# Kernel optimization log

Hardware: AMD Instinct MI355X
Metric: run time of the kernel (lower is better)

The kernel has to match this reference:

```python
import jax, jax.numpy as jnp
import numpy as np

B, T, V, D, E = 128, 50, 10000, 512, 2048


def setup_inputs() -> dict:
    key = jax.random.key(0)
    ks = jax.random.split(key, 14)
    s = 1.0 / np.sqrt(D)
    enc_out = jax.random.normal(ks[0], (B, E), jnp.float32)
    captions = jax.random.randint(ks[1], (B, T), 0, V)
    caplens = jax.random.randint(ks[2], (B, 1), 2, T + 1)
    caplens = caplens.at[0, 0].set(T)  # ensure max(caplens)-1 == T-1 (static shape)
    return {
        "enc_out": enc_out,
        "captions": captions,
        "caplens": caplens,
        "emb_W": jax.random.normal(ks[3], (V, D), jnp.float32),
        "W_ih": jax.random.uniform(ks[4], (4 * D, D), jnp.float32, -s, s),
        "W_hh": jax.random.uniform(ks[5], (4 * D, D), jnp.float32, -s, s),
        "b_ih": jax.random.uniform(ks[6], (4 * D,), jnp.float32, -s, s),
        "b_hh": jax.random.uniform(ks[7], (4 * D,), jnp.float32, -s, s),
        "fc_W": jax.random.uniform(ks[8], (V, D), jnp.float32, -s, s),
        "fc_b": jnp.zeros((V,), jnp.float32),
        "init_h_W": jax.random.uniform(ks[9], (D, E), jnp.float32, -s, s),
        "init_h_b": jnp.zeros((D,), jnp.float32),
        "init_c_W": jax.random.uniform(ks[10], (D, E), jnp.float32, -s, s),
        "init_c_b": jnp.zeros((D,), jnp.float32),
    }


def reference(enc_out, captions, caplens, emb_W, W_ih, W_hh, b_ih, b_hh,
              fc_W, fc_b, init_h_W, init_h_b, init_c_W, init_c_b):
    # Sort by caption length, descending (manual packing in the torch code).
    cl = caplens[:, 0]
    sort_idx = jnp.argsort(-cl)
    cl = cl[sort_idx]
    enc = enc_out[sort_idx]
    caps = captions[sort_idx]

    # init_states
    h0 = enc @ init_h_W.T + init_h_b  # [B, D]
    c0 = enc @ init_c_W.T + init_c_b

    emb = emb_W[caps]                  # [B, T, D] embedding gather
    dec_lens = cl - 1                  # decode lengths, max == T-1 by construction
    Tm = caps.shape[1] - 1             # static max timesteps

    # active-row mask per timestep: row b is active at step t iff t < dec_lens[b]
    masks = jnp.arange(Tm)[:, None] < dec_lens[None, :]   # [Tm, B]
    xs = jnp.moveaxis(emb[:, :Tm, :], 1, 0)               # [Tm, B, D]

    def step(carry, inp):
        h, c = carry
        x_t, m = inp                                      # [B,D], [B]
        gates = x_t @ W_ih.T + b_ih + h @ W_hh.T + b_hh   # [B, 4D]
        i, f, g, o = jnp.split(gates, 4, axis=-1)
        i = jax.nn.sigmoid(i)
        f = jax.nn.sigmoid(f)
        g = jnp.tanh(g)
        o = jax.nn.sigmoid(o)
        c_new = f * c + i * g
        h_new = o * jnp.tanh(c_new)
        mm = m[:, None]
        # inactive (shorter) rows keep their old state; torch never touches them
        h = jnp.where(mm, h_new, h)
        c = jnp.where(mm, c_new, c)
        # dropout in eval mode == identity; preds only written for active rows
        preds = jnp.where(mm, h_new @ fc_W.T + fc_b, 0.0)  # [B, V]
        return (h, c), preds

    (_, _), preds = jax.lax.scan(step, (h0, c0), (xs, masks))  # [Tm, B, V]
    predictions = jnp.moveaxis(preds, 0, 1)                    # [B, Tm, V]
    return predictions, caps, dec_lens, sort_idx
```

## Files before the change

### kernel.cpp

```cpp
#include <hip/hip_runtime.h>
#include <hip/hip_bf16.h>
#include <math.h>

typedef __attribute__((ext_vector_type(8))) short short8;
typedef __attribute__((ext_vector_type(4))) float f32x4;
typedef __attribute__((ext_vector_type(4))) unsigned short us4;
typedef unsigned short u16;
typedef unsigned long long u64;

#define TM 49
#define NV 10000
#define NLSTM 64
#define NFC 192
#define SMEM_BYTES 133120

__device__ __forceinline__ u16 f2bf(float f) {
    union { float f; unsigned u; } v; v.f = f;
    unsigned r = v.u + 0x7fffu + ((v.u >> 16) & 1u);
    return (u16)(r >> 16);
}
__device__ __forceinline__ float fsigm(float x) {
    return 1.0f / (1.0f + __expf(-x));
}
__device__ __forceinline__ float ftanh(float x) {
    float x2 = fminf(fmaxf(x + x, -30.0f), 30.0f);
    float e = __expf(x2);
    return (e - 1.0f) / (e + 1.0f);
}

__device__ __forceinline__ short8 ld_cp128(const u16* p) {
    short8 r;
    asm volatile("global_load_dwordx4 %0, %1, off sc0 sc1" : "=v"(r) : "v"(p));
    return r;
}
__device__ __forceinline__ void st_cp16(u16* p, unsigned v) {
    asm volatile("global_store_short %0, %1, off sc0 sc1" :: "v"(p), "v"(v) : "memory");
}
__device__ __forceinline__ void st_cp32f(float* p, float v) {
    asm volatile("global_store_dword %0, %1, off sc0 sc1" :: "v"(p), "v"(v) : "memory");
}
__device__ __forceinline__ unsigned ld_cp32_wait(const unsigned* p) {
    unsigned r;
    asm volatile("global_load_dword %0, %1, off sc0 sc1\n\ts_waitcnt vmcnt(0)"
                 : "=v"(r) : "v"(p) : "memory");
    return r;
}

__global__ __launch_bounds__(128) void k_sort(
    const int* __restrict__ caplens, const int* __restrict__ captions,
    const float* __restrict__ bih, const float* __restrict__ bhh,
    int* __restrict__ sidx, int* __restrict__ decl, int* __restrict__ capsS,
    float* __restrict__ bsum, float* __restrict__ out_tail,
    unsigned* __restrict__ slots, unsigned* __restrict__ xcnt,
    int* __restrict__ offs, int* __restrict__ rowmap, int* __restrict__ maskmap)
{
    __shared__ int s_cl[128];
    __shared__ int s_si[128];
    __shared__ int s_dl[128];
    __shared__ int s_n[49];
    __shared__ int s_off[50];
    __shared__ int s_moff[128];
    int tid = threadIdx.x;
    for (int k = tid; k < 256; k += 128)
        __hip_atomic_store(&slots[k], 0u, __ATOMIC_RELAXED, __HIP_MEMORY_SCOPE_AGENT);
    for (int k = tid; k < 1568; k += 128)
        __hip_atomic_store(&xcnt[k], 0u, __ATOMIC_RELAXED, __HIP_MEMORY_SCOPE_AGENT);
    int my = caplens[tid];
    s_cl[tid] = my;
    __syncthreads();
    int r = 0;
    for (int j = 0; j < 128; j++) {
        int cj = s_cl[j];
        if (cj > my || (cj == my && j < tid)) r++;
    }
    s_si[r] = tid;
    __syncthreads();
    int src = s_si[tid];
    sidx[tid] = src;
    int dl = s_cl[src] - 1;
    decl[tid] = dl;
    s_dl[tid] = dl;
    out_tail[6400 + tid] = (float)dl;
    out_tail[6528 + tid] = (float)src;
    for (int t = 0; t < 50; t++) {
        int tok = captions[src * 50 + t];
        capsS[tid * 50 + t] = tok;
        out_tail[tid * 50 + t] = (float)tok;
    }
    for (int k = tid; k < 2048; k += 128) bsum[k] = bih[k] + bhh[k];
    __syncthreads();
    if (tid < 49) {
        int c = 0;
        for (int b = 0; b < 128; b++) c += (s_dl[b] > tid);
        s_n[tid] = c;
    }
    __syncthreads();
    if (tid == 0) {
        int a = 0;
        for (int t = 0; t < 49; t++) { s_off[t] = a; a += s_n[t]; }
        s_off[49] = a;
        int m = 0;
        for (int b = 0; b < 128; b++) { s_moff[b] = m; m += 49 - s_dl[b]; }
    }
    __syncthreads();
    if (tid < 50) offs[tid] = s_off[tid];
    for (int t = 0; t < dl; t++) rowmap[s_off[t] + tid] = t * 128 + tid;
    int mo = s_moff[tid];
    for (int t = dl; t < 49; t++) maskmap[mo + (t - dl)] = tid * 49 + t;
}

__global__ __launch_bounds__(256) void k_cvt(
    const float* __restrict__ Wih, const float* __restrict__ Whh,
    const float* __restrict__ fcW, const float* __restrict__ ihW,
    const float* __restrict__ icW,
    u16* __restrict__ WihB, u16* __restrict__ WhhB,
    u16* __restrict__ fcWB, u16* __restrict__ WhcB)
{
    int idx = blockIdx.x * 256 + threadIdx.x;
    const float* src; u16* dst; int o;
    if (idx < 262144)        { src = Wih; dst = WihB; o = idx; }
    else if (idx < 524288)   { src = Whh; dst = WhhB; o = idx - 262144; }
    else if (idx < 1804288)  { src = fcW; dst = fcWB; o = idx - 524288; }
    else if (idx < 2066432)  { src = ihW; dst = WhcB; o = idx - 1804288; }
    else                     { src = icW; dst = WhcB + 1048576; o = idx - 2066432; }
    f32x4 v = *(const f32x4*)&src[(size_t)o * 4];
    us4 b = { f2bf(v.x), f2bf(v.y), f2bf(v.z), f2bf(v.w) };
    *(us4*)&dst[(size_t)o * 4] = b;
}

__global__ __launch_bounds__(256) void k_gather(
    const float* __restrict__ enc, const float* __restrict__ embW,
    const int* __restrict__ sidx, const int* __restrict__ capsS,
    u16* __restrict__ encB, u16* __restrict__ Xemb)
{
    int idx = blockIdx.x * 256 + threadIdx.x;
    if (idx < 65536) {
        int b = idx >> 9, k4 = idx & 511;
        f32x4 v = *(const f32x4*)&enc[(size_t)sidx[b] * 2048 + k4 * 4];
        us4 o = { f2bf(v.x), f2bf(v.y), f2bf(v.z), f2bf(v.w) };
        *(us4*)&encB[(size_t)b * 2048 + k4 * 4] = o;
    } else {
        int j = idx - 65536;
        int row = j >> 7, k4 = j & 127;
        int t = row >> 7, b = row & 127;
        int tok = capsS[b * 50 + t];
        f32x4 v = *(const f32x4*)&embW[(size_t)tok * 512 + k4 * 4];
        us4 o = { f2bf(v.x), f2bf(v.y), f2bf(v.z), f2bf(v.w) };
        *(us4*)&Xemb[(size_t)row * 512 + k4 * 4] = o;
    }
}

__device__ __forceinline__ void tile_gemm_plain(
    const u16* __restrict__ A, int lda, const u16* __restrict__ B, int ldb,
    int K, int tid, u16 (*As)[40], u16 (*Bs)[40], f32x4 acc[4][4])
{
    const int w = tid >> 6, l = tid & 63;
    const int wr = (w >> 1) * 64, wc = (w & 1) * 64;
    const int lr = l & 15, lg = l >> 4;
    for (int k0 = 0; k0 < K; k0 += 32) {
        __syncthreads();
        #pragma unroll
        for (int i = 0; i < 2; i++) {
            int L = tid * 8 + i * 2048;
            int r = L >> 5, c = L & 31;
            *(short8*)&As[r][c] = *(const short8*)&A[(size_t)r * lda + k0 + c];
            *(short8*)&Bs[r][c] = *(const short8*)&B[(size_t)r * ldb + k0 + c];
        }
        __syncthreads();
        short8 af[4], bfr[4];
        #pragma unroll
        for (int m = 0; m < 4; m++) af[m] = *(const short8*)&As[wr + m * 16 + lr][lg * 8];
        #pragma unroll
        for (int n = 0; n < 4; n++) bfr[n] = *(const short8*)&Bs[wc + n * 16 + lr][lg * 8];
        #pragma unroll
        for (int m = 0; m < 4; m++)
            #pragma unroll
            for (int n = 0; n < 4; n++)
                acc[m][n] = __builtin_amdgcn_mfma_f32_16x16x32_bf16(af[m], bfr[n], acc[m][n], 0, 0, 0);
    }
}

__global__ __launch_bounds__(256, 1) void lstm_fc(
    const u16* __restrict__ Whh, float* __restrict__ X,
    u16* __restrict__ hb0, u16* __restrict__ hb1,
    u16* __restrict__ HnewC,
    const int* __restrict__ decl, unsigned* __restrict__ slots,
    unsigned* __restrict__ xcnt,
    const int* __restrict__ offs, const int* __restrict__ rowmap,
    const int* __restrict__ maskmap,
    const u16* __restrict__ fcWB, const float* __restrict__ fcb,
    const u16* __restrict__ encB, const u16* __restrict__ WhcB,
    const u16* __restrict__ WihB, const u16* __restrict__ Xemb,
    const float* __restrict__ bsum,
    const float* __restrict__ ihb, const float* __restrict__ icb,
    float* __restrict__ out)
{
    extern __shared__ char smem[];
    const int tid = threadIdx.x;
    const int wg = blockIdx.x;

    if (wg < NLSTM) {
        u16 (*As)[520] = (u16(*)[520])smem;
        u16 (*Bsi)[520] = (u16(*)[520])(smem + 33280);
        const int rb = wg >> 4, cb = wg & 15;
        const int w = tid >> 6, l = tid & 63;
        const int hi = w >> 1, lo = w & 1;
        const int lr = l & 15, lg = l >> 4;
        unsigned* cnt = slots + rb * 32;

        const int col = cb * 32 + lo * 16 + lr;
        int rowg[4];
        #pragma unroll
        for (int i = 0; i < 4; i++) rowg[i] = rb * 32 + hi * 16 + lg * 4 + i;

        f32x4 acch = {}, accc = {};
        for (int kq = 0; kq < 4; kq++) {
            __syncthreads();
            #pragma unroll
            for (int i = 0; i < 8; i++) {
                int L = tid * 8 + i * 2048;
                int r = L >> 9, cc = L & 511;
                *(short8*)&As[r][cc] =
                    *(const short8*)&encB[(size_t)(rb * 32 + r) * 2048 + kq * 512 + cc];
                *(short8*)&Bsi[r][cc] =
                    *(const short8*)&WhcB[(size_t)(cb * 32 + r) * 2048 + kq * 512 + cc];
            }
            __syncthreads();
            #pragma unroll
            for (int kk = 0; kk < 16; kk++) {
                short8 a = *(const short8*)&As[hi * 16 + lr][kk * 32 + lg * 8];
                short8 b = *(const short8*)&Bsi[lo * 16 + lr][kk * 32 + lg * 8];
                acch = __builtin_amdgcn_mfma_f32_16x16x32_bf16(a, b, acch, 0, 0, 0);
            }
            __syncthreads();
            #pragma unroll
            for (int i = 0; i < 8; i++) {
                int L = tid * 8 + i * 2048;
                int r = L >> 9, cc = L & 511;
                *(short8*)&Bsi[r][cc] =
                    *(const short8*)&WhcB[(size_t)(512 + cb * 32 + r) * 2048 + kq * 512 + cc];
            }
            __syncthreads();
            #pragma unroll
            for (int kk = 0; kk < 16; kk++) {
                short8 a = *(const short8*)&As[hi * 16 + lr][kk * 32 + lg * 8];
                short8 b = *(const short8*)&Bsi[lo * 16 + lr][kk * 32 + lg * 8];
                accc = __builtin_amdgcn_mfma_f32_16x16x32_bf16(a, b, accc, 0, 0, 0);
            }
        }

        int edec[4];
        f32x4 creg;
        us4 hreg;
        #pragma unroll
        for (int i = 0; i < 4; i++) {
            edec[i] = decl[rowg[i]];
            creg[i] = accc[i] + icb[col];
            hreg[i] = f2bf(acch[i] + ihb[col]);
            st_cp16(&hb0[(size_t)rowg[i] * 512 + col], (unsigned)hreg[i]);
        }
        asm volatile("s_waitcnt vmcnt(0)" ::: "memory");
        __syncthreads();
        if (tid == 0) atomicAdd(cnt, 1u);

        short8 bq[4][16];
        #pragma unroll
        for (int q = 0; q < 4; q++) {
            const u16* base = &Whh[(size_t)(q * 512 + cb * 32 + lo * 16 + lr) * 512 + lg * 8];
            #pragma unroll
            for (int kk = 0; kk < 16; kk++)
                bq[q][kk] = *(const short8*)&base[kk * 32];
        }
        #pragma unroll
        for (int q = 0; q < 4; q++)
            #pragma unroll
            for (int kk = 0; kk < 16; kk++)
                asm volatile("" : "+v"(bq[q][kk]));

        for (int t = 0; t < TM; t++) {
            const u16* hin = (t & 1) ? hb1 : hb0;
            u16* hout = (t & 1) ? hb0 : hb1;

            {
                unsigned tgt_h = 16u * (unsigned)(t + 1);
                if (tid == 0) {
                    while (ld_cp32_wait(cnt) < tgt_h) __builtin_amdgcn_s_sleep(1);
                } else if (tid == 64) {
                    while (ld_cp32_wait(&xcnt[t * 32]) < 16u) __builtin_amdgcn_s_sleep(1);
                }
                __syncthreads();
            }

            float xq[4][4];
            #pragma unroll
            for (int q = 0; q < 4; q++)
                #pragma unroll
                for (int i = 0; i < 4; i++)
                    xq[q][i] = X[(size_t)t * 262144 + (size_t)rowg[i] * 2048 + q * 512 + col];
            int offt = offs[t];

            short8 tmp[8];
            #pragma unroll
            for (int i = 0; i < 8; i++) {
                int L = i * 256 + tid;
                int r = L >> 6, cc = (L & 63) * 8;
                tmp[i] = ld_cp128(&hin[(size_t)(rb * 32 + r) * 512 + cc]);
            }
            asm volatile("s_waitcnt vmcnt(0)" ::: "memory");
            __builtin_amdgcn_sched_barrier(0);
            #pragma unroll
            for (int i = 0; i < 8; i++) {
                int L = i * 256 + tid;
                int r = L >> 6, cc = (L & 63) * 8;
                *(short8*)&As[r][cc] = tmp[i];
            }
            __syncthreads();

            f32x4 acc[4] = {};
            #pragma unroll
            for (int kk = 0; kk < 16; kk++) {
                short8 a = *(const short8*)&As[hi * 16 + lr][kk * 32 + lg * 8];
                acc[0] = __builtin_amdgcn_mfma_f32_16x16x32_bf16(a, bq[0][kk], acc[0], 0, 0, 0);
                acc[1] = __builtin_amdgcn_mfma_f32_16x16x32_bf16(a, bq[1][kk], acc[1], 0, 0, 0);
                acc[2] = __builtin_amdgcn_mfma_f32_16x16x32_bf16(a, bq[2][kk], acc[2], 0, 0, 0);
                acc[3] = __builtin_amdgcn_mfma_f32_16x16x32_bf16(a, bq[3][kk], acc[3], 0, 0, 0);
            }

            #pragma unroll
            for (int i = 0; i < 4; i++) {
                int act = (t < edec[i]);
                float iv = fsigm(acc[0][i] + xq[0][i]);
                float fv = fsigm(acc[1][i] + xq[1][i]);
                float gv = ftanh(acc[2][i] + xq[2][i]);
                float ov = fsigm(acc[3][i] + xq[3][i]);
                float cn = fv * creg[i] + iv * gv;
                float hn_f = ov * ftanh(cn);
                if (act) {
                    creg[i] = cn;
                    hreg[i] = f2bf(hn_f);
                }
                st_cp16(&hout[(size_t)rowg[i] * 512 + col], (unsigned)hreg[i]);
                if (act)
                    st_cp16(&HnewC[(size_t)(offt + rowg[i]) * 512 + col], (unsigned)hreg[i]);
            }

            asm volatile("s_waitcnt vmcnt(0)" ::: "memory");
            __syncthreads();
            if (tid == 0) atomicAdd(cnt, 1u);
        }
    } else {
        const int f = wg - NLSTM;
        const int w = tid >> 6, l = tid & 63;
        const int wr = (w >> 1) * 64, wc = (w & 1) * 64;
        const int lr = l & 15, lg = l >> 4;

        int nrC = offs[49];
        int nzero = 6272 - nrC;
        int nzjobs = (nzero + 1) >> 1;
        int nrt = (nrC + 127) >> 7;

        {
            u16 (*As)[40] = (u16(*)[40])smem;
            u16 (*Bs)[40] = (u16(*)[40])(smem + 10240);
            for (int j = f; j < 784; j += NFC) {
                int tt = j >> 4, cbx = j & 15;
                f32x4 acc[4][4] = {};
                tile_gemm_plain(Xemb + (size_t)tt * 128 * 512, 512,
                                WihB + (size_t)cbx * 128 * 512, 512,
                                512, tid, As, Bs, acc);
                #pragma unroll
                for (int m = 0; m < 4; m++)
                    #pragma unroll
                    for (int n = 0; n < 4; n++)
                        #pragma unroll
                        for (int i = 0; i < 4; i++) {
                            int row = wr + m * 16 + lg * 4 + i;
                            int colg = cbx * 128 + wc + n * 16 + lr;
                            st_cp32f(&X[(size_t)tt * 262144 + (size_t)row * 2048 + colg],
                                     acc[m][n][i] + bsum[colg]);
                        }
                asm volatile("s_waitcnt vmcnt(0)" ::: "memory");
                __syncthreads();
                if (tid == 0) atomicAdd(&xcnt[tt * 32], 1u);
            }
        }

        for (int j = f; j < nzjobs; j += NFC) {
            int z = j * 2;
            #pragma unroll
            for (int rr = 0; rr < 2; rr++) {
                if (z + rr < nzero) {
                    float* dst = out + (size_t)maskmap[z + rr] * 10000;
                    f32x4 zv = {};
                    for (int i = tid; i < 2500; i += 256) *(f32x4*)&dst[i * 4] = zv;
                }
            }
        }

        int c = f % 79;
        int sub = f / 79;
        int gsize = (c < 34) ? 3 : 2;

        u16 (*BT)[520] = (u16(*)[520])smem;
        __syncthreads();
        #pragma unroll
        for (int i = 0; i < 32; i++) {
            int L = i * 256 + tid;
            int r = L >> 6, cc = (L & 63) * 8;
            int gn = c * 128 + r;
            short8 b = {};
            if (gn < NV) b = *(const short8*)&fcWB[(size_t)gn * 512 + cc];
            *(short8*)&BT[r][cc] = b;
        }
        __syncthreads();

        for (int rt = sub; rt < nrt; rt += gsize) {
            int lastrow = min(rt * 128 + 127, nrC - 1);
            int tmax = rowmap[lastrow] >> 7;
            unsigned tgt = 16u * (unsigned)(tmax + 2);
            if (tid < 4) {
                const unsigned* cp = slots + tid * 32;
                while (ld_cp32_wait(cp) < tgt) __builtin_amdgcn_s_sleep(1);
            }
            __syncthreads();

            f32x4 acc[4][4] = {};
            #pragma unroll
            for (int ks = 0; ks < 16; ks++) {
                short8 af[4], bfr[4];
                #pragma unroll
                for (int m = 0; m < 4; m++) {
                    int gr = rt * 128 + wr + m * 16 + lr;
                    short8 a = {};
                    if (gr < nrC)
                        a = *(const short8*)&HnewC[(size_t)gr * 512 + ks * 32 + lg * 8];
                    af[m] = a;
                }
                #pragma unroll
                for (int n = 0; n < 4; n++)
                    bfr[n] = *(const short8*)&BT[wc + n * 16 + lr][ks * 32 + lg * 8];
                #pragma unroll
                for (int m = 0; m < 4; m++)
                    #pragma unroll
                    for (int n = 0; n < 4; n++)
                        acc[m][n] = __builtin_amdgcn_mfma_f32_16x16x32_bf16(af[m], bfr[n], acc[m][n], 0, 0, 0);
            }

            #pragma unroll
            for (int m = 0; m < 4; m++)
                #pragma unroll
                for (int n = 0; n < 4; n++)
                    #pragma unroll
                    for (int i = 0; i < 4; i++) {
                        int row = rt * 128 + wr + m * 16 + lg * 4 + i;
                        int colg = c * 128 + wc + n * 16 + lr;
                        if (row < nrC && colg < NV) {
                            int map = rowmap[row];
                            int b = map & 127, tt = map >> 7;
                            out[(size_t)(b * 49 + tt) * 10000 + colg] =
                                acc[m][n][i] + fcb[colg];
                        }
                    }
        }
    }
}

extern "C" void kernel_launch(void* const* d_in, const int* in_sizes, int n_in,
                              void* d_out, int out_size, void* d_ws, size_t ws_size,
                              hipStream_t stream) {
    const float* enc      = (const float*)d_in[0];
    const int*   captions = (const int*)d_in[1];
    const int*   caplens  = (const int*)d_in[2];
    const float* embW     = (const float*)d_in[3];
    const float* Wih      = (const float*)d_in[4];
    const float* Whh      = (const float*)d_in[5];
    const float* bih      = (const float*)d_in[6];
    const float* bhh      = (const float*)d_in[7];
    const float* fcW      = (const float*)d_in[8];
    const float* fcb      = (const float*)d_in[9];
    const float* ihW      = (const float*)d_in[10];
    const float* ihb      = (const float*)d_in[11];
    const float* icW      = (const float*)d_in[12];
    const float* icb      = (const float*)d_in[13];
    float* out = (float*)d_out;

    char* ws = (char*)d_ws;
    u16*   WihB = (u16*)(ws + 0);
    u16*   WhhB = (u16*)(ws + 2097152);
    u16*   fcWB = (u16*)(ws + 4194304);
    u16*   WhcB = (u16*)(ws + 14434304);
    u16*   encB = (u16*)(ws + 18628608);
    u16*   Xemb = (u16*)(ws + 19152896);
    float* X    = (float*)(ws + 25575424);
    u16*   HnewC= (u16*)(ws + 76955648);
    u16*   hb0  = (u16*)(ws + 83378176);
    u16*   hb1  = (u16*)(ws + 83509248);
    int*   sidx = (int*)(ws + 83902464);
    int*   decl = (int*)(ws + 83902976);
    int*   capsS= (int*)(ws + 83903488);
    float* bsum = (float*)(ws + 83929088);
    unsigned* slots = (unsigned*)(ws + 83937280);
    int*   offs   = (int*)(ws + 83938304);
    int*   rowmap = (int*)(ws + 83938560);
    int*   maskmap= (int*)(ws + 83963648);
    unsigned* xcnt = (unsigned*)(ws + 83988736);

    k_sort<<<1, 128, 0, stream>>>(caplens, captions, bih, bhh, sidx, decl, capsS, bsum,
                                  out + 62720000, slots, xcnt, offs, rowmap, maskmap);
    k_cvt<<<9096, 256, 0, stream>>>(Wih, Whh, fcW, ihW, icW, WihB, WhhB, fcWB, WhcB);
    k_gather<<<3392, 256, 0, stream>>>(enc, embW, sidx, capsS, encB, Xemb);
    lstm_fc<<<NLSTM + NFC, 256, SMEM_BYTES, stream>>>(
        WhhB, X, hb0, hb1, HnewC, decl, slots, xcnt, offs, rowmap, maskmap,
        fcWB, fcb, encB, WhcB, WihB, Xemb, bsum, ihb, icb, out);
}
```

Baseline: 367.8 us.

## Overlap zero-fill of masked prediction rows with waits for LSTM progress

The FC workgroups no longer zero all inactive output rows up front. They fill those rows one at a time while polling the LSTM progress counters, so the zeroing happens during spin-waits, and any rows left over are zeroed after the FC tiles finish. The poll now goes through a small shared-memory array with two barriers per iteration, and the sleep is longer when there is nothing left to zero. Output stores for both the zeros and the logits switch to nontemporal stores to reduce cache pollution. The extra barriers add some polling overhead, and zero-fill work may land unevenly across workgroups.

```diff
diff --git a/kernel.cpp b/kernel.cpp
--- a/kernel.cpp
+++ b/kernel.cpp
@@ -12,7 +12,7 @@
 #define NV 10000
 #define NLSTM 64
 #define NFC 192
-#define SMEM_BYTES 133120
+#define SMEM_BYTES 133184
 
 __device__ __forceinline__ u16 f2bf(float f) {
     union { float f; unsigned u; } v; v.f = f;
@@ -356,7 +356,6 @@
 
         int nrC = offs[49];
         int nzero = 6272 - nrC;
-        int nzjobs = (nzero + 1) >> 1;
         int nrt = (nrC + 127) >> 7;
 
         {
@@ -385,23 +384,12 @@
             }
         }
 
-        for (int j = f; j < nzjobs; j += NFC) {
-            int z = j * 2;
-            #pragma unroll
-            for (int rr = 0; rr < 2; rr++) {
-                if (z + rr < nzero) {
-                    float* dst = out + (size_t)maskmap[z + rr] * 10000;
-                    f32x4 zv = {};
-                    for (int i = tid; i < 2500; i += 256) *(f32x4*)&dst[i * 4] = zv;
-                }
-            }
-        }
-
         int c = f % 79;
         int sub = f / 79;
         int gsize = (c < 34) ? 3 : 2;
 
         u16 (*BT)[520] = (u16(*)[520])smem;
+        unsigned* s_cnt = (unsigned*)(smem + 133120);
         __syncthreads();
         #pragma unroll
         for (int i = 0; i < 32; i++) {
@@ -414,15 +402,30 @@
         }
         __syncthreads();
 
+        int znext = f;
+        f32x4 zv = {};
+
         for (int rt = sub; rt < nrt; rt += gsize) {
             int lastrow = min(rt * 128 + 127, nrC - 1);
             int tmax = rowmap[lastrow] >> 7;
             unsigned tgt = 16u * (unsigned)(tmax + 2);
-            if (tid < 4) {
-                const unsigned* cp = slots + tid * 32;
-                while (ld_cp32_wait(cp) < tgt) __builtin_amdgcn_s_sleep(1);
-            }
-            __syncthreads();
+
+            while (true) {
+                if (tid < 4) s_cnt[tid] = ld_cp32_wait(slots + tid * 32);
+                __syncthreads();
+                bool rdy = (s_cnt[0] >= tgt) && (s_cnt[1] >= tgt) &&
+                           (s_cnt[2] >= tgt) && (s_cnt[3] >= tgt);
+                __syncthreads();
+                if (rdy) break;
+                if (znext < nzero) {
+                    float* dst = out + (size_t)maskmap[znext] * 10000;
+                    for (int i = tid; i < 2500; i += 256)
+                        __builtin_nontemporal_store(zv, (f32x4*)&dst[i * 4]);
+                    znext += NFC;
+                } else {
+                    __builtin_amdgcn_s_sleep(16);
+                }
+            }
 
             f32x4 acc[4][4] = {};
             #pragma unroll
@@ -457,10 +460,18 @@
                         if (row < nrC && colg < NV) {
                             int map = rowmap[row];
                             int b = map & 127, tt = map >> 7;
-                            out[(size_t)(b * 49 + tt) * 10000 + colg] =
-                                acc[m][n][i] + fcb[colg];
+                            __builtin_nontemporal_store(
+                                acc[m][n][i] + fcb[colg],
+                                &out[(size_t)(b * 49 + tt) * 10000 + colg]);
                         }
                     }
+        }
+
+        while (znext < nzero) {
+            float* dst = out + (size_t)maskmap[znext] * 10000;
+            for (int i = tid; i < 2500; i += 256)
+                __builtin_nontemporal_store(zv, (f32x4*)&dst[i * 4]);
+            znext += NFC;
         }
     }
 }
```

Result: faster. 350.2 us (-4.8%).
